# Kernel optimization log

Measured on AMD Instinct MI355X. Metric: run time of the kernel, lower is better.

Reference implementation:

```python
import jax, jax.numpy as jnp
import numpy as np

NHEAD = 16
HEAD_DIM = 64
EMBED_DIM = NHEAD * HEAD_DIM  # 1024
U, R, L, M = 2048, 256, 1024, 512


def setup_inputs() -> dict:
    key = jax.random.key(0)
    ks = jax.random.split(key, 11)
    D = EMBED_DIM
    inp = {
        "utterance": jax.random.normal(ks[0], (U, 1, D), jnp.float32),
        "right_context": jax.random.normal(ks[1], (R, 1, D), jnp.float32),
        "memory": jax.random.normal(ks[2], (M, 1, D), jnp.float32),
        "left_context_key": jax.random.normal(ks[3], (L, 1, D), jnp.float32),
        "left_context_val": jax.random.normal(ks[4], (L, 1, D), jnp.float32),
        "Wq": jax.random.normal(ks[5], (D, D), jnp.float32) * 0.02,
        "bq": jax.random.normal(ks[6], (D,), jnp.float32) * 0.02,
        "Wkv": jax.random.normal(ks[7], (2 * D, D), jnp.float32) * 0.02,
        "bkv": jax.random.normal(ks[8], (2 * D,), jnp.float32) * 0.02,
        "Wo": jax.random.normal(ks[9], (D, D), jnp.float32) * 0.02,
        "bo": jax.random.normal(ks[10], (D,), jnp.float32) * 0.02,
    }
    return inp


def reference(utterance, right_context, memory, left_context_key, left_context_val,
              Wq, bq, Wkv, bkv, Wo, bo):
    D = EMBED_DIM
    scaling = HEAD_DIM ** (-0.5)

    # query = Linear([right_context; utterance])  -> (Q, 1, D), Q = R + U
    q_in = jnp.concatenate([right_context, utterance], axis=0)
    query = q_in @ Wq.T + bq

    # key/value = Linear([memory; right_context; utterance]) split in two
    kv_in = jnp.concatenate([memory, right_context, utterance], axis=0)
    kv = kv_in @ Wkv.T + bkv  # (M+R+U, 1, 2D)
    k_new, v_new = kv[..., :D], kv[..., D:]

    # insert cached left-context key/value after [memory; right_context]
    key = jnp.concatenate([k_new[: M + R], left_context_key, k_new[M + R:]], axis=0)
    value = jnp.concatenate([v_new[: M + R], left_context_val, v_new[M + R:]], axis=0)

    Q = U + R
    KV = M + R + L + U
    # (T, 1, D) -> (nhead, T, head_dim)
    q = query.reshape(Q, NHEAD, HEAD_DIM).transpose(1, 0, 2)
    k = key.reshape(KV, NHEAD, HEAD_DIM).transpose(1, 0, 2)
    v = value.reshape(KV, NHEAD, HEAD_DIM).transpose(1, 0, 2)

    weights = jnp.einsum("hqd,hkd->hqk", q * scaling, k)  # (nhead, Q, KV)
    probs = jax.nn.softmax(weights, axis=-1)
    attn = jnp.einsum("hqk,hkd->hqd", probs, v)  # (nhead, Q, head_dim)

    attn = attn.transpose(1, 0, 2).reshape(Q, D)[:, None, :]  # (Q, 1, D)
    out = attn @ Wo.T + bo
    return out, key, value
```

## Files before the change

### kernel.cpp

```cpp
#include <hip/hip_runtime.h>
#include <hip/hip_bf16.h>

#define EMBED   1024
#define NHEADS  16
#define HDIM    64
#define U_LEN   2048
#define R_LEN   256
#define L_LEN   1024
#define M_LEN   512
#define Q_LEN   (U_LEN + R_LEN)
#define KV_LEN  (M_LEN + R_LEN + L_LEN + U_LEN)
#define X_ROWS  (M_LEN + R_LEN + U_LEN)
#define NPART   6
#define KV_PART (KV_LEN / NPART)

typedef __attribute__((ext_vector_type(8))) short short8;
typedef __attribute__((ext_vector_type(4))) float f32x4;
typedef __attribute__((ext_vector_type(16))) float f32x16;

#define QSCALE 0.180336880f

__device__ __forceinline__ void gl2lds16(const __hip_bfloat16* g, __hip_bfloat16* l) {
  __builtin_amdgcn_global_load_lds(
      (const __attribute__((address_space(1))) unsigned int*)g,
      (__attribute__((address_space(3))) unsigned int*)l, 16, 0, 0);
}

__device__ __forceinline__ unsigned pack_bf16(float a, float b) {
  unsigned ua = __builtin_bit_cast(unsigned, a) + 0x8000u;
  unsigned ub = __builtin_bit_cast(unsigned, b) + 0x8000u;
  return (ua >> 16) | (ub & 0xFFFF0000u);
}

__global__ __launch_bounds__(256) void prep_kernel(
    const float* __restrict__ mem, const float* __restrict__ rc,
    const float* __restrict__ utt, const float* __restrict__ lk,
    const float* __restrict__ lv, const float* __restrict__ Wq,
    const float* __restrict__ Wkv, const float* __restrict__ Wo,
    __hip_bfloat16* __restrict__ X, __hip_bfloat16* __restrict__ WB,
    __hip_bfloat16* __restrict__ WoB,
    float* __restrict__ key_out, float* __restrict__ val_out,
    __hip_bfloat16* __restrict__ k_bf, __hip_bfloat16* __restrict__ v_bf) {
  int b = blockIdx.x, tid = threadIdx.x;
  if (b < 2816) {
    int row = b, col = tid * 4;
    const float* src;
    if (row < M_LEN)              src = mem + row * EMBED;
    else if (row < M_LEN + R_LEN) src = rc + (row - M_LEN) * EMBED;
    else                          src = utt + (row - M_LEN - R_LEN) * EMBED;
    float4 v = *reinterpret_cast<const float4*>(src + col);
    __hip_bfloat16* d = X + (size_t)row * EMBED + col;
    d[0] = __float2bfloat16(v.x); d[1] = __float2bfloat16(v.y);
    d[2] = __float2bfloat16(v.z); d[3] = __float2bfloat16(v.w);
  } else if (b < 6912) {
    const float* src; __hip_bfloat16* dst;
    int blk;
    if (b < 3840)      { src = Wq;  dst = WB;                blk = b - 2816; }
    else if (b < 5888) { src = Wkv; dst = WB + 1024 * 1024;  blk = b - 3840; }
    else               { src = Wo;  dst = WoB;               blk = b - 5888; }
    int idx = blk * 1024 + tid * 4;
    float4 v = *reinterpret_cast<const float4*>(src + idx);
    dst[idx + 0] = __float2bfloat16(v.x);
    dst[idx + 1] = __float2bfloat16(v.y);
    dst[idx + 2] = __float2bfloat16(v.z);
    dst[idx + 3] = __float2bfloat16(v.w);
  } else {
    int row = b - 6912, c0 = tid * 4;
    int orow = 768 + row;
    float4 kv4 = *reinterpret_cast<const float4*>(lk + row * EMBED + c0);
    float4 vv4 = *reinterpret_cast<const float4*>(lv + row * EMBED + c0);
    *reinterpret_cast<float4*>(key_out + (size_t)orow * EMBED + c0) = kv4;
    *reinterpret_cast<float4*>(val_out + (size_t)orow * EMBED + c0) = vv4;
    __hip_bfloat16* kd = k_bf + (size_t)orow * EMBED + c0;
    __hip_bfloat16* vd = v_bf + (size_t)orow * EMBED + c0;
    kd[0] = __float2bfloat16(kv4.x); kd[1] = __float2bfloat16(kv4.y);
    kd[2] = __float2bfloat16(kv4.z); kd[3] = __float2bfloat16(kv4.w);
    vd[0] = __float2bfloat16(vv4.x); vd[1] = __float2bfloat16(vv4.y);
    vd[2] = __float2bfloat16(vv4.z); vd[3] = __float2bfloat16(vv4.w);
  }
}

__global__ __launch_bounds__(256) void transpose_kernel(
    const unsigned short* __restrict__ v_bf, unsigned short* __restrict__ vT) {
  __shared__ unsigned short T[64][72];
  int kt = blockIdx.x * 64, d0 = blockIdx.y * 64;
  int t = threadIdx.x;
  int r = t >> 3, c = (t & 7) * 8;
#pragma unroll
  for (int half = 0; half < 2; half++) {
    int kv = r + half * 32;
    short8 v = *reinterpret_cast<const short8*>(v_bf + (size_t)(kt + kv) * EMBED + d0 + c);
#pragma unroll
    for (int j = 0; j < 8; j++) T[c + j][kv] = (unsigned short)v[j];
  }
  __syncthreads();
#pragma unroll
  for (int half = 0; half < 2; half++) {
    int d = r + half * 32;
    *reinterpret_cast<short8*>(vT + (size_t)(d0 + d) * KV_LEN + kt + c) =
        *reinterpret_cast<const short8*>(&T[d][c]);
  }
}

__global__ __launch_bounds__(256) void gemm_qkv(
    const __hip_bfloat16* __restrict__ A, const __hip_bfloat16* __restrict__ B,
    const float* __restrict__ bq, const float* __restrict__ bkv,
    float* __restrict__ key_out, float* __restrict__ val_out,
    __hip_bfloat16* __restrict__ q_bf, __hip_bfloat16* __restrict__ k_bf,
    __hip_bfloat16* __restrict__ v_bf) {
  __shared__ __align__(16) __hip_bfloat16 As[128 * 64];
  __shared__ __align__(16) __hip_bfloat16 Bs[64 * 64];
  const int K = EMBED;
  int tid = threadIdx.x;
  int wave = tid >> 6, lane = tid & 63, quad = lane >> 4, l16 = lane & 15;
  int wm = wave >> 1, wn = wave & 1;
  int mbase = blockIdx.y * 128, nbase = blockIdx.x * 64;

  if (nbase < 1024 && mbase + 128 <= 512) return;

  int srow = tid >> 3;
  int scol = ((tid & 7) ^ (srow & 7)) * 8;
  const __hip_bfloat16* aG = A + (size_t)(mbase + srow) * K + scol;
  const __hip_bfloat16* bG = B + (size_t)(nbase + srow) * K + scol;
  int swz = l16 & 7;

  f32x4 acc[4][2] = {};
  for (int kt = 0; kt < K; kt += 64) {
    gl2lds16(aG + kt, As + tid * 8);
    gl2lds16(aG + (size_t)32 * K + kt, As + (tid + 256) * 8);
    gl2lds16(aG + (size_t)64 * K + kt, As + (tid + 512) * 8);
    gl2lds16(aG + (size_t)96 * K + kt, As + (tid + 768) * 8);
    gl2lds16(bG + kt, Bs + tid * 8);
    gl2lds16(bG + (size_t)32 * K + kt, Bs + (tid + 256) * 8);
    __syncthreads();
#pragma unroll
    for (int ks = 0; ks < 2; ks++) {
      short8 af[4], bfr[2];
#pragma unroll
      for (int i = 0; i < 4; i++)
        af[i] = *reinterpret_cast<const short8*>(
            As + (wm * 64 + i * 16 + l16) * 64 + ((ks * 4 + quad) ^ swz) * 8);
#pragma unroll
      for (int j = 0; j < 2; j++)
        bfr[j] = *reinterpret_cast<const short8*>(
            Bs + (wn * 32 + j * 16 + l16) * 64 + ((ks * 4 + quad) ^ swz) * 8);
#pragma unroll
      for (int i = 0; i < 4; i++)
#pragma unroll
        for (int j = 0; j < 2; j++)
          acc[i][j] = __builtin_amdgcn_mfma_f32_16x16x32_bf16(af[i], bfr[j], acc[i][j], 0, 0, 0);
    }
    __syncthreads();
  }

#pragma unroll
  for (int i = 0; i < 4; i++) {
    int rb = mbase + wm * 64 + i * 16 + quad * 4;
#pragma unroll
    for (int j = 0; j < 2; j++) {
      int cg = nbase + wn * 32 + j * 16 + l16;
      float bv = (cg < 1024) ? bq[cg] : bkv[cg - 1024];
#pragma unroll
      for (int reg = 0; reg < 4; reg++) {
        int rg = rb + reg;
        float val = acc[i][j][reg] + bv;
        if (cg < 1024) {
          if (rg >= 512)
            q_bf[(size_t)(rg - 512) * 1024 + cg] = __float2bfloat16(val * QSCALE);
        } else {
          int orow = (rg < 768) ? rg : rg + 1024;
          if (cg < 2048) {
            int cc = cg - 1024;
            key_out[(size_t)orow * 1024 + cc] = val;
            k_bf[(size_t)orow * 1024 + cc] = __float2bfloat16(val);
          } else {
            int cc = cg - 2048;
            val_out[(size_t)orow * 1024 + cc] = val;
            v_bf[(size_t)orow * 1024 + cc] = __float2bfloat16(val);
          }
        }
      }
    }
  }
}

__global__ __launch_bounds__(256) void gemm_out(
    const __hip_bfloat16* __restrict__ A, const __hip_bfloat16* __restrict__ B,
    float* __restrict__ partial) {
  __shared__ __align__(16) __hip_bfloat16 As[64 * 64];
  __shared__ __align__(16) __hip_bfloat16 Bs[64 * 64];
  const int K = EMBED, N = EMBED;
  int tid = threadIdx.x;
  int wave = tid >> 6, lane = tid & 63, quad = lane >> 4, l16 = lane & 15;
  int wm = wave >> 1, wn = wave & 1;
  int mbase = blockIdx.y * 64, nbase = blockIdx.x * 64;
  int kbase = blockIdx.z * 512;
  float* outp = partial + (size_t)blockIdx.z * Q_LEN * EMBED;

  int srow = tid >> 3;
  int scol = ((tid & 7) ^ (srow & 7)) * 8;
  const __hip_bfloat16* aG = A + (size_t)(mbase + srow) * K + kbase + scol;
  const __hip_bfloat16* bG = B + (size_t)(nbase + srow) * K + kbase + scol;
  int swz = l16 & 7;

  f32x4 acc[2][2] = {};
  for (int kt = 0; kt < 512; kt += 64) {
    gl2lds16(aG + kt, As + tid * 8);
    gl2lds16(aG + (size_t)32 * K + kt, As + (tid + 256) * 8);
    gl2lds16(bG + kt, Bs + tid * 8);
    gl2lds16(bG + (size_t)32 * K + kt, Bs + (tid + 256) * 8);
    __syncthreads();
#pragma unroll
    for (int ks = 0; ks < 2; ks++) {
      short8 af[2], bfr[2];
#pragma unroll
      for (int i = 0; i < 2; i++)
        af[i] = *reinterpret_cast<const short8*>(
            As + (wm * 32 + i * 16 + l16) * 64 + ((ks * 4 + quad) ^ swz) * 8);
#pragma unroll
      for (int j = 0; j < 2; j++)
        bfr[j] = *reinterpret_cast<const short8*>(
            Bs + (wn * 32 + j * 16 + l16) * 64 + ((ks * 4 + quad) ^ swz) * 8);
#pragma unroll
      for (int i = 0; i < 2; i++)
#pragma unroll
        for (int j = 0; j < 2; j++)
          acc[i][j] = __builtin_amdgcn_mfma_f32_16x16x32_bf16(af[i], bfr[j], acc[i][j], 0, 0, 0);
    }
    __syncthreads();
  }

#pragma unroll
  for (int i = 0; i < 2; i++) {
    int rb = mbase + wm * 32 + i * 16 + quad * 4;
#pragma unroll
    for (int j = 0; j < 2; j++) {
      int cg = nbase + wn * 32 + j * 16 + l16;
#pragma unroll
      for (int reg = 0; reg < 4; reg++)
        outp[(size_t)(rb + reg) * N + cg] = acc[i][j][reg];
    }
  }
}

__global__ __launch_bounds__(256) void reduce_out_kernel(
    const float* __restrict__ partial, const float* __restrict__ bias,
    float* __restrict__ outf) {
  int row = blockIdx.x, c = threadIdx.x * 4;
  float4 p0 = *reinterpret_cast<const float4*>(partial + (size_t)row * EMBED + c);
  float4 p1 = *reinterpret_cast<const float4*>(partial + (size_t)(Q_LEN + row) * EMBED + c);
  float4 bv = *reinterpret_cast<const float4*>(bias + c);
  float4 o;
  o.x = p0.x + p1.x + bv.x; o.y = p0.y + p1.y + bv.y;
  o.z = p0.z + p1.z + bv.z; o.w = p0.w + p1.w + bv.w;
  *reinterpret_cast<float4*>(outf + (size_t)row * EMBED + c) = o;
}

__global__ __launch_bounds__(256, 4) void attn_kernel(
    const __hip_bfloat16* __restrict__ q_bf, const __hip_bfloat16* __restrict__ k_bf,
    const __hip_bfloat16* __restrict__ vT,
    __hip_bfloat16* __restrict__ o_part, float* __restrict__ lsum) {
  __shared__ __align__(16) __hip_bfloat16 Ks[64][72];
  __shared__ __align__(16) __hip_bfloat16 VTs[64][72];
  int tid = threadIdx.x;
  int w = tid >> 6, lane = tid & 63, l31 = lane & 31, h2 = lane >> 5;
  int h = blockIdx.y, part = blockIdx.z;
  int qbase = blockIdx.x * 128;
  int qg = qbase + w * 32 + l31;

  short8 Qf[4];
#pragma unroll
  for (int ks = 0; ks < 4; ks++)
    Qf[ks] = *reinterpret_cast<const short8*>(
        q_bf + (size_t)qg * EMBED + h * HDIM + ks * 16 + h2 * 8);

  f32x16 ot[2] = {};
  float l_run = 0.f;

  int sr = tid >> 3, sc = (tid & 7) * 8;
  const int kv0 = part * KV_PART;

  for (int kt = kv0; kt < kv0 + KV_PART; kt += 64) {
#pragma unroll
    for (int half = 0; half < 2; half++) {
      int r = sr + half * 32;
      *reinterpret_cast<short8*>(&Ks[r][sc]) =
          *reinterpret_cast<const short8*>(k_bf + (size_t)(kt + r) * EMBED + h * HDIM + sc);
      *reinterpret_cast<short8*>(&VTs[r][sc]) =
          *reinterpret_cast<const short8*>(vT + (size_t)(h * HDIM + r) * KV_LEN + kt + sc);
    }
    __syncthreads();

#pragma unroll
    for (int kvs = 0; kvs < 2; kvs++) {
      f32x16 s = {};
#pragma unroll
      for (int ks = 0; ks < 4; ks++) {
        short8 ak = *reinterpret_cast<const short8*>(&Ks[kvs * 32 + l31][ks * 16 + h2 * 8]);
        s = __builtin_amdgcn_mfma_f32_32x32x16_bf16(ak, Qf[ks], s, 0, 0, 0);
      }
      unsigned u[4][2];
#pragma unroll
      for (int g = 0; g < 4; g++) {
        float p0 = exp2f(s[4 * g + 0]), p1 = exp2f(s[4 * g + 1]);
        float p2 = exp2f(s[4 * g + 2]), p3 = exp2f(s[4 * g + 3]);
        l_run += (p0 + p1) + (p2 + p3);
        u[g][0] = pack_bf16(p0, p1);
        u[g][1] = pack_bf16(p2, p3);
      }
#pragma unroll
      for (int half = 0; half < 2; half++) {
        int c = kvs * 2 + half;
        int gA = 2 * half, gB = 2 * half + 1;
        unsigned s0 = h2 ? u[gA][0] : u[gB][0];
        unsigned s1 = h2 ? u[gA][1] : u[gB][1];
        unsigned r0 = __shfl_xor(s0, 32, 64);
        unsigned r1 = __shfl_xor(s1, 32, 64);
        uint4 fr;
        fr.x = h2 ? r0 : u[gA][0];
        fr.y = h2 ? r1 : u[gA][1];
        fr.z = h2 ? u[gB][0] : r0;
        fr.w = h2 ? u[gB][1] : r1;
        short8 pf = __builtin_bit_cast(short8, fr);
#pragma unroll
        for (int ds = 0; ds < 2; ds++) {
          short8 av = *reinterpret_cast<const short8*>(&VTs[ds * 32 + l31][c * 16 + h2 * 8]);
          ot[ds] = __builtin_amdgcn_mfma_f32_32x32x16_bf16(av, pf, ot[ds], 0, 0, 0);
        }
      }
    }
    __syncthreads();
  }

  l_run += __shfl_xor(l_run, 32, 64);
  float inv = 1.0f / l_run;

  size_t orow = (size_t)part * Q_LEN + qg;
#pragma unroll
  for (int ds = 0; ds < 2; ds++)
#pragma unroll
    for (int g = 0; g < 4; g++) {
      uint2 pk;
      pk.x = pack_bf16(ot[ds][4 * g + 0] * inv, ot[ds][4 * g + 1] * inv);
      pk.y = pack_bf16(ot[ds][4 * g + 2] * inv, ot[ds][4 * g + 3] * inv);
      *reinterpret_cast<uint2*>(
          o_part + orow * 1024 + h * HDIM + ds * 32 + g * 8 + h2 * 4) = pk;
    }
  if (lane < 32)
    lsum[orow * NHEADS + h] = l_run;
}

__global__ __launch_bounds__(256) void merge_kernel(
    const __hip_bfloat16* __restrict__ o_part, const float* __restrict__ lsum,
    __hip_bfloat16* __restrict__ attn_bf) {
  int q = blockIdx.x;
  int c = threadIdx.x * 4;
  int h = c >> 6;
  float wt[NPART], L = 0.f;
#pragma unroll
  for (int p = 0; p < NPART; p++) {
    wt[p] = lsum[((size_t)p * Q_LEN + q) * NHEADS + h];
    L += wt[p];
  }
  float invL = 1.0f / L;
  float acc[4] = {0.f, 0.f, 0.f, 0.f};
#pragma unroll
  for (int p = 0; p < NPART; p++) {
    __hip_bfloat16 v[4];
    *reinterpret_cast<uint2*>(v) =
        *reinterpret_cast<const uint2*>(o_part + ((size_t)p * Q_LEN + q) * 1024 + c);
#pragma unroll
    for (int j = 0; j < 4; j++) acc[j] += wt[p] * __bfloat162float(v[j]);
  }
  uint2 pk;
  pk.x = pack_bf16(acc[0] * invL, acc[1] * invL);
  pk.y = pack_bf16(acc[2] * invL, acc[3] * invL);
  *reinterpret_cast<uint2*>(attn_bf + (size_t)q * 1024 + c) = pk;
}


extern "C" void kernel_launch(void* const* d_in, const int* in_sizes, int n_in,
                              void* d_out, int out_size, void* d_ws, size_t ws_size,
                              hipStream_t stream) {
  const float* utt = (const float*)d_in[0];
  const float* rc  = (const float*)d_in[1];
  const float* mem = (const float*)d_in[2];
  const float* lk  = (const float*)d_in[3];
  const float* lv  = (const float*)d_in[4];
  const float* Wq  = (const float*)d_in[5];
  const float* bq  = (const float*)d_in[6];
  const float* Wkv = (const float*)d_in[7];
  const float* bkv = (const float*)d_in[8];
  const float* Wo  = (const float*)d_in[9];
  const float* bo  = (const float*)d_in[10];

  float* out_f   = (float*)d_out;
  float* key_out = out_f + Q_LEN * EMBED;
  float* val_out = key_out + KV_LEN * EMBED;

  char* ws = (char*)d_ws;
  size_t off = 0;
  __hip_bfloat16* X_bf   = (__hip_bfloat16*)(ws + off); off += (size_t)X_ROWS * EMBED * 2;
  __hip_bfloat16* WB_bf  = (__hip_bfloat16*)(ws + off); off += (size_t)3 * EMBED * EMBED * 2;
  __hip_bfloat16* Wo_bf  = (__hip_bfloat16*)(ws + off); off += (size_t)EMBED * EMBED * 2;
  __hip_bfloat16* q_bf   = (__hip_bfloat16*)(ws + off); off += (size_t)Q_LEN * EMBED * 2;
  __hip_bfloat16* k_bf   = (__hip_bfloat16*)(ws + off); off += (size_t)KV_LEN * EMBED * 2;
  __hip_bfloat16* vT_bf  = (__hip_bfloat16*)(ws + off); off += (size_t)EMBED * KV_LEN * 2;
  __hip_bfloat16* o_part = (__hip_bfloat16*)(ws + off); off += (size_t)NPART * Q_LEN * EMBED * 2;
  __hip_bfloat16* attn_bf = X_bf;
  float* lsum = (float*)WB_bf;
  __hip_bfloat16* v_bf = o_part;
  float* out_partial = (float*)q_bf;
  (void)off; (void)ws_size; (void)in_sizes; (void)n_in; (void)out_size;

  prep_kernel<<<7936, 256, 0, stream>>>(mem, rc, utt, lk, lv, Wq, Wkv, Wo,
                                        X_bf, WB_bf, Wo_bf,
                                        key_out, val_out, k_bf, v_bf);
  gemm_qkv<<<dim3(3 * EMBED / 64, X_ROWS / 128), 256, 0, stream>>>(
      X_bf, WB_bf, bq, bkv, key_out, val_out, q_bf, k_bf, v_bf);
  transpose_kernel<<<dim3(KV_LEN / 64, EMBED / 64), 256, 0, stream>>>(
      (const unsigned short*)v_bf, (unsigned short*)vT_bf);
  attn_kernel<<<dim3(Q_LEN / 128, NHEADS, NPART), 256, 0, stream>>>(
      q_bf, k_bf, vT_bf, o_part, lsum);
  merge_kernel<<<Q_LEN, 256, 0, stream>>>(o_part, lsum, attn_bf);
  gemm_out<<<dim3(EMBED / 64, Q_LEN / 64, 2), 256, 0, stream>>>(
      attn_bf, Wo_bf, out_partial);
  reduce_out_kernel<<<Q_LEN, 256, 0, stream>>>(out_partial, bo, out_f);
}
```

Baseline: 243.4 us.

## Prefetch K/V tiles into registers, remap attention blocks per XCD, use native cvt/permlane ops

The attention kernel now loads the next K/V tile into registers while computing the current one, so global loads overlap with MFMA work. The grid is flattened and remapped so that blocks sharing a (part, head) pair land on the same XCD, which should improve L2 reuse. It also uses the hardware v_cvt_pk_bf16_f32 for packing (round-to-nearest-even, slightly different from the old rounding), permlane32_swap in place of the shuffle-based exchange, the raw exp2 builtin, s_setprio around the MFMA sections, and raises the launch-bounds occupancy target from 4 to 6. The extra prefetch registers combined with the higher occupancy target could cause spills.

```diff
diff --git a/kernel.cpp b/kernel.cpp
--- a/kernel.cpp
+++ b/kernel.cpp
@@ -27,9 +27,22 @@
 }
 
 __device__ __forceinline__ unsigned pack_bf16(float a, float b) {
-  unsigned ua = __builtin_bit_cast(unsigned, a) + 0x8000u;
-  unsigned ub = __builtin_bit_cast(unsigned, b) + 0x8000u;
-  return (ua >> 16) | (ub & 0xFFFF0000u);
+  unsigned r;
+  asm("v_cvt_pk_bf16_f32 %0, %1, %2" : "=v"(r) : "v"(a), "v"(b));
+  return r;
+}
+
+__device__ __forceinline__ void plane_swap(unsigned a, unsigned b, int h2,
+                                           unsigned& lo, unsigned& hi) {
+#if __has_builtin(__builtin_amdgcn_permlane32_swap)
+  auto r = __builtin_amdgcn_permlane32_swap(a, b, false, false);
+  lo = r[0]; hi = r[1];
+#else
+  unsigned s0 = h2 ? a : b;
+  unsigned r0 = __shfl_xor(s0, 32, 64);
+  lo = h2 ? r0 : a;
+  hi = h2 ? b : r0;
+#endif
 }
 
 __global__ __launch_bounds__(256) void prep_kernel(
@@ -256,7 +269,7 @@
   *reinterpret_cast<float4*>(outf + (size_t)row * EMBED + c) = o;
 }
 
-__global__ __launch_bounds__(256, 4) void attn_kernel(
+__global__ __launch_bounds__(256, 6) void attn_kernel(
     const __hip_bfloat16* __restrict__ q_bf, const __hip_bfloat16* __restrict__ k_bf,
     const __hip_bfloat16* __restrict__ vT,
     __hip_bfloat16* __restrict__ o_part, float* __restrict__ lsum) {
@@ -264,8 +277,13 @@
   __shared__ __align__(16) __hip_bfloat16 VTs[64][72];
   int tid = threadIdx.x;
   int w = tid >> 6, lane = tid & 63, l31 = lane & 31, h2 = lane >> 5;
-  int h = blockIdx.y, part = blockIdx.z;
-  int qbase = blockIdx.x * 128;
+
+  int lid = blockIdx.x;
+  int xcd = lid & 7, sfl = lid >> 3;
+  int gi = sfl / 18, j = sfl - gi * 18;
+  int g = gi * 8 + xcd;
+  int part = g >> 4, h = g & 15;
+  int qbase = j * 128;
   int qg = qbase + w * 32 + l31;
 
   short8 Qf[4];
@@ -280,56 +298,74 @@
   int sr = tid >> 3, sc = (tid & 7) * 8;
   const int kv0 = part * KV_PART;
 
+  short8 kr[2], vr[2];
+#pragma unroll
+  for (int half = 0; half < 2; half++) {
+    int r = sr + half * 32;
+    kr[half] = *reinterpret_cast<const short8*>(
+        k_bf + (size_t)(kv0 + r) * EMBED + h * HDIM + sc);
+    vr[half] = *reinterpret_cast<const short8*>(
+        vT + (size_t)(h * HDIM + r) * KV_LEN + kv0 + sc);
+  }
+
   for (int kt = kv0; kt < kv0 + KV_PART; kt += 64) {
+    __syncthreads();
 #pragma unroll
     for (int half = 0; half < 2; half++) {
       int r = sr + half * 32;
-      *reinterpret_cast<short8*>(&Ks[r][sc]) =
-          *reinterpret_cast<const short8*>(k_bf + (size_t)(kt + r) * EMBED + h * HDIM + sc);
-      *reinterpret_cast<short8*>(&VTs[r][sc]) =
-          *reinterpret_cast<const short8*>(vT + (size_t)(h * HDIM + r) * KV_LEN + kt + sc);
-    }
-    __syncthreads();
+      *reinterpret_cast<short8*>(&Ks[r][sc]) = kr[half];
+      *reinterpret_cast<short8*>(&VTs[r][sc]) = vr[half];
+    }
+    __syncthreads();
+    if (kt + 64 < kv0 + KV_PART) {
+#pragma unroll
+      for (int half = 0; half < 2; half++) {
+        int r = sr + half * 32;
+        kr[half] = *reinterpret_cast<const short8*>(
+            k_bf + (size_t)(kt + 64 + r) * EMBED + h * HDIM + sc);
+        vr[half] = *reinterpret_cast<const short8*>(
+            vT + (size_t)(h * HDIM + r) * KV_LEN + kt + 64 + sc);
+      }
+    }
 
 #pragma unroll
     for (int kvs = 0; kvs < 2; kvs++) {
       f32x16 s = {};
+      __builtin_amdgcn_s_setprio(1);
 #pragma unroll
       for (int ks = 0; ks < 4; ks++) {
         short8 ak = *reinterpret_cast<const short8*>(&Ks[kvs * 32 + l31][ks * 16 + h2 * 8]);
         s = __builtin_amdgcn_mfma_f32_32x32x16_bf16(ak, Qf[ks], s, 0, 0, 0);
       }
+      __builtin_amdgcn_s_setprio(0);
       unsigned u[4][2];
 #pragma unroll
-      for (int g = 0; g < 4; g++) {
-        float p0 = exp2f(s[4 * g + 0]), p1 = exp2f(s[4 * g + 1]);
-        float p2 = exp2f(s[4 * g + 2]), p3 = exp2f(s[4 * g + 3]);
+      for (int gq = 0; gq < 4; gq++) {
+        float p0 = __builtin_amdgcn_exp2f(s[4 * gq + 0]);
+        float p1 = __builtin_amdgcn_exp2f(s[4 * gq + 1]);
+        float p2 = __builtin_amdgcn_exp2f(s[4 * gq + 2]);
+        float p3 = __builtin_amdgcn_exp2f(s[4 * gq + 3]);
         l_run += (p0 + p1) + (p2 + p3);
-        u[g][0] = pack_bf16(p0, p1);
-        u[g][1] = pack_bf16(p2, p3);
+        u[gq][0] = pack_bf16(p0, p1);
+        u[gq][1] = pack_bf16(p2, p3);
       }
 #pragma unroll
       for (int half = 0; half < 2; half++) {
         int c = kvs * 2 + half;
         int gA = 2 * half, gB = 2 * half + 1;
-        unsigned s0 = h2 ? u[gA][0] : u[gB][0];
-        unsigned s1 = h2 ? u[gA][1] : u[gB][1];
-        unsigned r0 = __shfl_xor(s0, 32, 64);
-        unsigned r1 = __shfl_xor(s1, 32, 64);
         uint4 fr;
-        fr.x = h2 ? r0 : u[gA][0];
-        fr.y = h2 ? r1 : u[gA][1];
-        fr.z = h2 ? u[gB][0] : r0;
-        fr.w = h2 ? u[gB][1] : r1;
+        plane_swap(u[gA][0], u[gB][0], h2, fr.x, fr.z);
+        plane_swap(u[gA][1], u[gB][1], h2, fr.y, fr.w);
         short8 pf = __builtin_bit_cast(short8, fr);
+        __builtin_amdgcn_s_setprio(1);
 #pragma unroll
         for (int ds = 0; ds < 2; ds++) {
           short8 av = *reinterpret_cast<const short8*>(&VTs[ds * 32 + l31][c * 16 + h2 * 8]);
           ot[ds] = __builtin_amdgcn_mfma_f32_32x32x16_bf16(av, pf, ot[ds], 0, 0, 0);
         }
+        __builtin_amdgcn_s_setprio(0);
       }
     }
-    __syncthreads();
   }
 
   l_run += __shfl_xor(l_run, 32, 64);
@@ -339,12 +375,12 @@
 #pragma unroll
   for (int ds = 0; ds < 2; ds++)
 #pragma unroll
-    for (int g = 0; g < 4; g++) {
+    for (int gq = 0; gq < 4; gq++) {
       uint2 pk;
-      pk.x = pack_bf16(ot[ds][4 * g + 0] * inv, ot[ds][4 * g + 1] * inv);
-      pk.y = pack_bf16(ot[ds][4 * g + 2] * inv, ot[ds][4 * g + 3] * inv);
+      pk.x = pack_bf16(ot[ds][4 * gq + 0] * inv, ot[ds][4 * gq + 1] * inv);
+      pk.y = pack_bf16(ot[ds][4 * gq + 2] * inv, ot[ds][4 * gq + 3] * inv);
       *reinterpret_cast<uint2*>(
-          o_part + orow * 1024 + h * HDIM + ds * 32 + g * 8 + h2 * 4) = pk;
+          o_part + orow * 1024 + h * HDIM + ds * 32 + gq * 8 + h2 * 4) = pk;
     }
   if (lane < 32)
     lsum[orow * NHEADS + h] = l_run;
@@ -370,7 +406,7 @@
     *reinterpret_cast<uint2*>(v) =
         *reinterpret_cast<const uint2*>(o_part + ((size_t)p * Q_LEN + q) * 1024 + c);
 #pragma unroll
-    for (int j = 0; j < 4; j++) acc[j] += wt[p] * __bfloat162float(v[j]);
+    for (int jj = 0; jj < 4; jj++) acc[jj] += wt[p] * __bfloat162float(v[jj]);
   }
   uint2 pk;
   pk.x = pack_bf16(acc[0] * invL, acc[1] * invL);
@@ -420,7 +456,7 @@
       X_bf, WB_bf, bq, bkv, key_out, val_out, q_bf, k_bf, v_bf);
   transpose_kernel<<<dim3(KV_LEN / 64, EMBED / 64), 256, 0, stream>>>(
       (const unsigned short*)v_bf, (unsigned short*)vT_bf);
-  attn_kernel<<<dim3(Q_LEN / 128, NHEADS, NPART), 256, 0, stream>>>(
+  attn_kernel<<<dim3((Q_LEN / 128) * NHEADS * NPART), 256, 0, stream>>>(
       q_bf, k_bf, vT_bf, o_part, lsum);
   merge_kernel<<<Q_LEN, 256, 0, stream>>>(o_part, lsum, attn_bf);
   gemm_out<<<dim3(EMBED / 64, Q_LEN / 64, 2), 256, 0, stream>>>(
```

After: 305.6 us. 25.6% more time.
